# Optimization experiments

Measured on AMD Instinct MI355X. Metric: run time of the kernel, lower is better.

## Reference

```python
import jax, jax.numpy as jnp
import numpy as np

NSAMPLE = 64
RADIUS = 0.05
HMIN = -0.02
HMAX_LIST = (0.01, 0.02, 0.03, 0.04)
BN_EPS = 1e-5
MLP_DIMS = (3, 64, 128, 256)


def setup_inputs() -> dict:
    key = jax.random.key(0)
    ks = jax.random.split(key, 16)
    B, S, N = 2, 1024, 20000
    # points and seeds in a [0,0.5]^3 box so 0.05-radius cylinders are non-empty
    seed_xyz = jax.random.uniform(ks[0], (B, S, 3), dtype=jnp.float32) * 0.5
    pointcloud = jax.random.uniform(ks[1], (B, N, 3), dtype=jnp.float32) * 0.5
    m = jax.random.normal(ks[2], (B, S, 3, 3), dtype=jnp.float32)
    vp_rot, _ = jnp.linalg.qr(m)  # proper-ish random rotations per seed
    inp = {"seed_xyz": seed_xyz, "pointcloud": pointcloud, "vp_rot": vp_rot}
    for i in range(3):
        cin, cout = MLP_DIMS[i], MLP_DIMS[i + 1]
        inp[f"w{i+1}"] = jax.random.normal(ks[3 + i], (cout, cin), dtype=jnp.float32) * (1.0 / np.sqrt(cin))
        inp[f"gamma{i+1}"] = 1.0 + 0.1 * jax.random.normal(ks[6 + i], (cout,), dtype=jnp.float32)
        inp[f"beta{i+1}"] = 0.1 * jax.random.normal(ks[9 + i], (cout,), dtype=jnp.float32)
        inp[f"mean{i+1}"] = 0.1 * jax.random.normal(ks[12 + i], (cout,), dtype=jnp.float32)
        inp[f"var{i+1}"] = jax.random.uniform(ks[15], (cout,), minval=0.5, maxval=1.5, dtype=jnp.float32)
    return inp


def _cylinder_group(rel_rot, hmax):
    # rel_rot: (B, S, N, 3) point coords relative to each seed, in the seed (approach) frame.
    # Cylinder axis = x (approach vector): keep points with hmin < x < hmax and y^2+z^2 < r^2.
    N = rel_rot.shape[2]
    x, y, z = rel_rot[..., 0], rel_rot[..., 1], rel_rot[..., 2]
    mask = (y * y + z * z < RADIUS * RADIUS) & (x > HMIN) & (x < hmax)  # (B,S,N)
    # first NSAMPLE valid indices (ascending), padded with the first valid index (0 if none)
    score = jnp.where(mask, jnp.arange(N, dtype=jnp.int32), N)
    neg_vals, _ = jax.lax.top_k(-score, NSAMPLE)
    idx = -neg_vals  # (B,S,NSAMPLE), value N marks missing
    first = jnp.where(idx[..., :1] >= N, 0, idx[..., :1])
    idx = jnp.where(idx >= N, first, idx)
    return jnp.take_along_axis(rel_rot, idx[..., None], axis=2)  # (B,S,NSAMPLE,3)


def _bn_relu(h, gamma, beta, mean, var):
    inv = gamma / jnp.sqrt(var + BN_EPS)
    s = inv[None, :, None, None]
    b = (beta - mean * inv)[None, :, None, None]
    return jax.nn.relu(h * s + b)


def _forward(seed_xyz, pointcloud, vp_rot, layers):
    B, S, _ = seed_xyz.shape
    D = len(HMAX_LIST)
    rel = pointcloud[:, None, :, :] - seed_xyz[:, :, None, :]        # (B,S,N,3)
    rel_rot = jnp.einsum('bsnc,bscd->bsnd', rel, vp_rot)             # rotate into seed frame (rel @ rot)
    grouped = jnp.stack([_cylinder_group(rel_rot, h) for h in HMAX_LIST], axis=2)  # (B,S,D,ns,3)
    feat = jnp.transpose(grouped, (0, 4, 1, 2, 3)).reshape(B, 3, S * D, NSAMPLE)   # (B,3,S*D,ns)
    for (w, g, be, m, v) in layers:
        feat = _bn_relu(jnp.einsum('oc,bcpn->bopn', w, feat), g, be, m, v)
    vp = jnp.max(feat, axis=-1)                                       # max-pool over nsample
    return vp.reshape(B, -1, S, D)                                    # (B,256,S,D)


def reference(seed_xyz, pointcloud, vp_rot,
              w1, gamma1, beta1, mean1, var1,
              w2, gamma2, beta2, mean2, var2,
              w3, gamma3, beta3, mean3, var3):
    layers = [(w1, gamma1, beta1, mean1, var1),
              (w2, gamma2, beta2, mean2, var2),
              (w3, gamma3, beta3, mean3, var3)]
    return _forward(seed_xyz, pointcloud, vp_rot, layers)
```

## Files before the change

### kernel.cpp

```cpp
#include <hip/hip_runtime.h>

#define NPTS   20000
#define NCHUNK 313

typedef __bf16 bf16x8 __attribute__((ext_vector_type(8)));
typedef float  f32x4  __attribute__((ext_vector_type(4)));

__device__ __forceinline__ unsigned short f2b(float f) {
    __bf16 h = (__bf16)f;
    union { __bf16 h; unsigned short s; } u; u.h = h; return u.s;
}
__device__ __forceinline__ unsigned int pk2(float a, float b) {
    return (unsigned int)f2b(a) | ((unsigned int)f2b(b) << 16);
}
__device__ __forceinline__ bf16x8 pack8v(const float* __restrict__ f) {
    f32x4 a = *(const f32x4*)(f);
    f32x4 c = *(const f32x4*)(f + 4);
    union { unsigned short s[8]; bf16x8 v; } u;
    #pragma unroll
    for (int i = 0; i < 4; ++i) u.s[i]     = f2b(a[i]);
    #pragma unroll
    for (int i = 0; i < 4; ++i) u.s[i + 4] = f2b(c[i]);
    return u.v;
}

#define WS_BINNED  0
#define WS_COUNTS  640000
#define WS_OFFSETS 644096
#define WS_CURSORS 648192

__global__ void zero_kernel(unsigned int* __restrict__ counts,
                            unsigned int* __restrict__ cursors)
{
    int t = blockIdx.x * 256 + threadIdx.x;
    if (t < 1024) { counts[t] = 0; cursors[t] = 0; }
}

__global__ __launch_bounds__(256)
void count_kernel(const float* __restrict__ pointcloud,
                  unsigned int* __restrict__ counts)
{
    int t = blockIdx.x * 256 + threadIdx.x;
    if (t >= 2 * NPTS) return;
    int b = (t >= NPTS) ? 1 : 0;
    const float* p = pointcloud + t * 3;
    int cx = min(7, (int)(p[0] * 16.0f));
    int cy = min(7, (int)(p[1] * 16.0f));
    int cz = min(7, (int)(p[2] * 16.0f));
    int cid = (cz * 8 + cy) * 8 + cx;
    atomicAdd(&counts[b * 512 + cid], 1u);
}

__global__ __launch_bounds__(512)
void prefix_kernel(const unsigned int* __restrict__ counts,
                   unsigned int* __restrict__ offsets,
                   unsigned int* __restrict__ cursors)
{
    __shared__ unsigned int sdat[512];
    int b = blockIdx.x;
    int tid = threadIdx.x;
    unsigned int v = counts[b * 512 + tid];
    sdat[tid] = v;
    __syncthreads();
    #pragma unroll
    for (int off = 1; off < 512; off <<= 1) {
        unsigned int t = 0;
        if (tid >= off) t = sdat[tid - off];
        __syncthreads();
        sdat[tid] += t;
        __syncthreads();
    }
    unsigned int base = b * NPTS + (sdat[tid] - v);
    offsets[b * 512 + tid] = base;
    cursors[b * 512 + tid] = base;
}

__global__ __launch_bounds__(256)
void scatter_kernel(const float* __restrict__ pointcloud,
                    unsigned int* __restrict__ cursors,
                    float4* __restrict__ binned)
{
    int t = blockIdx.x * 256 + threadIdx.x;
    if (t >= 2 * NPTS) return;
    int b = (t >= NPTS) ? 1 : 0;
    int i = t - b * NPTS;
    const float* p = pointcloud + t * 3;
    float x = p[0], y = p[1], z = p[2];
    int cx = min(7, (int)(x * 16.0f));
    int cy = min(7, (int)(y * 16.0f));
    int cz = min(7, (int)(z * 16.0f));
    int cid = (cz * 8 + cy) * 8 + cx;
    unsigned int slot = atomicAdd(&cursors[b * 512 + cid], 1u);
    binned[slot] = make_float4(x, y, z, __int_as_float(i));
}

struct __align__(16) SMemF {
    union {
        struct {
            unsigned int bm[4][640];
            int cstart[64];
            int ccnt[64];
        } a;
        struct {
            unsigned short h1[64][72];
            unsigned short h2[64][136];
        } b;
    } u;
    int    idxs[4][64];
    float  X[4][64][3];
    float2 sb2[128];
    float2 sb3[256];
    float  w1e[64][3];
    float  b1e[64];
};

__global__ __launch_bounds__(256, 2)
void fused_kernel(const float* __restrict__ seed_xyz,
                  const float* __restrict__ pointcloud,
                  const float* __restrict__ vp_rot,
                  const unsigned int* __restrict__ counts,
                  const unsigned int* __restrict__ offsets,
                  const float4* __restrict__ binned,
                  const float* __restrict__ w1,
                  const float* __restrict__ g1,  const float* __restrict__ be1,
                  const float* __restrict__ mn1, const float* __restrict__ vr1,
                  const float* __restrict__ w2,
                  const float* __restrict__ g2,  const float* __restrict__ be2,
                  const float* __restrict__ mn2, const float* __restrict__ vr2,
                  const float* __restrict__ w3,
                  const float* __restrict__ g3,  const float* __restrict__ be3,
                  const float* __restrict__ mn3, const float* __restrict__ vr3,
                  float* __restrict__ out)
{
    __shared__ SMemF sm;
    const int tid = threadIdx.x;
    const int wv  = tid >> 6;
    const int ln  = tid & 63;
    const int q   = ln >> 4;
    const int l15 = ln & 15;

    const int blk = blockIdx.x;
    const int i8  = blk >> 3;
    const int s   = (blk & 7) * 128 + (i8 & 127);
    const int b   = i8 >> 7;
    const int bs  = b * 1024 + s;

    {
        float inv = g3[tid] / sqrtf(vr3[tid] + 1e-5f);
        sm.sb3[tid] = make_float2(inv, be3[tid] - mn3[tid] * inv);
    }
    if (tid < 128) {
        float inv = g2[tid] / sqrtf(vr2[tid] + 1e-5f);
        sm.sb2[tid] = make_float2(inv, be2[tid] - mn2[tid] * inv);
    }
    if (tid < 64) {
        float inv = g1[tid] / sqrtf(vr1[tid] + 1e-5f);
        sm.w1e[tid][0] = inv * w1[tid*3+0];
        sm.w1e[tid][1] = inv * w1[tid*3+1];
        sm.w1e[tid][2] = inv * w1[tid*3+2];
        sm.b1e[tid]    = be1[tid] - mn1[tid] * inv;
    }

    {
        unsigned int* bmp = &sm.u.a.bm[0][0];
        #pragma unroll
        for (int i = 0; i < 10; ++i) bmp[tid + i * 256] = 0;
    }

    const float sx = seed_xyz[bs*3+0];
    const float sy = seed_xyz[bs*3+1];
    const float sz = seed_xyz[bs*3+2];
    const float R00 = vp_rot[bs*9+0], R01 = vp_rot[bs*9+1], R02 = vp_rot[bs*9+2];
    const float R10 = vp_rot[bs*9+3], R11 = vp_rot[bs*9+4], R12 = vp_rot[bs*9+5];
    const float R20 = vp_rot[bs*9+6], R21 = vp_rot[bs*9+7], R22 = vp_rot[bs*9+8];

    const int lx = max(0, (int)floorf((sx - 0.066f) * 16.f));
    const int hx = min(7, (int)floorf((sx + 0.066f) * 16.f));
    const int ly = max(0, (int)floorf((sy - 0.066f) * 16.f));
    const int hy = min(7, (int)floorf((sy + 0.066f) * 16.f));
    const int lz = max(0, (int)floorf((sz - 0.066f) * 16.f));
    const int hz = min(7, (int)floorf((sz + 0.066f) * 16.f));
    const int nx = hx - lx + 1, ny = hy - ly + 1, nz = hz - lz + 1;
    const int ncell = nx * ny * nz;

    if (tid < ncell) {
        int cz = lz + tid / (nx * ny);
        int rem = tid % (nx * ny);
        int cy = ly + rem / nx;
        int cx = lx + rem % nx;
        int cid = (cz * 8 + cy) * 8 + cx;
        sm.u.a.cstart[tid] = (int)offsets[b * 512 + cid];
        sm.u.a.ccnt[tid]   = (int)counts [b * 512 + cid];
    }
    __syncthreads();

    {
        #pragma clang fp contract(off)
        for (int k = wv; k < ncell; k += 4) {
            const int base = sm.u.a.cstart[k];
            const int cnt  = sm.u.a.ccnt[k];
            for (int i = ln; i < cnt; i += 64) {
                float4 pt = binned[base + i];
                float rx = pt.x - sx, ry = pt.y - sy, rz = pt.z - sz;
                float x = (rx*R00 + ry*R10) + rz*R20;
                float y = (rx*R01 + ry*R11) + rz*R21;
                float z = (rx*R02 + ry*R12) + rz*R22;
                if (((y*y + z*z) < 0.0025f) && (x > -0.02f) && (x < 0.04f)) {
                    int n = __float_as_int(pt.w);
                    unsigned int bit = 1u << (n & 31);
                    int wi = n >> 5;
                    if (x < 0.01f) atomicOr(&sm.u.a.bm[0][wi], bit);
                    if (x < 0.02f) atomicOr(&sm.u.a.bm[1][wi], bit);
                    if (x < 0.03f) atomicOr(&sm.u.a.bm[2][wi], bit);
                    atomicOr(&sm.u.a.bm[3][wi], bit);
                }
            }
        }
    }
    __syncthreads();

    {
        const int d = wv;
        int carry = 0;
        for (int r = 0; r < 5 && carry < 64; ++r) {
            int c = r*64 + ln;
            unsigned long long w = 0ULL;
            if (c < NCHUNK)
                w = ((unsigned long long)sm.u.a.bm[d][2*c+1] << 32)
                  |  (unsigned long long)sm.u.a.bm[d][2*c];
            int wc = __popcll(w);
            int incl = wc;
            #pragma unroll
            for (int off = 1; off < 64; off <<= 1) {
                int t = __shfl_up(incl, off);
                if (ln >= off) incl += t;
            }
            int rank  = carry + incl - wc;
            int total = __shfl(incl, 63);
            while (w && rank < 64) {
                int bp = __builtin_ctzll(w);
                w &= w - 1;
                sm.idxs[d][rank] = c*64 + bp;
                ++rank;
            }
            carry += total;
        }
        int cnt = carry < 64 ? carry : 64;
        int first = (cnt > 0) ? sm.idxs[d][0] : 0;
        if (ln >= cnt) sm.idxs[d][ln] = first;
    }
    __syncthreads();

    {
        #pragma clang fp contract(off)
        int n = sm.idxs[wv][ln];
        const float* p = pointcloud + (b*NPTS + n)*3;
        float rx = p[0] - sx, ry = p[1] - sy, rz = p[2] - sz;
        sm.X[wv][ln][0] = (rx*R00 + ry*R10) + rz*R20;
        sm.X[wv][ln][1] = (rx*R01 + ry*R11) + rz*R21;
        sm.X[wv][ln][2] = (rx*R02 + ry*R12) + rz*R22;
    }

    bf16x8 aw2[2][2], aw3[4][4];
    #pragma unroll
    for (int m = 0; m < 2; ++m)
        #pragma unroll
        for (int kk = 0; kk < 2; ++kk)
            aw2[m][kk] = pack8v(w2 + ((wv*2+m)*16 + l15)*64 + kk*32 + q*8);
    #pragma unroll
    for (int m = 0; m < 4; ++m)
        #pragma unroll
        for (int kk = 0; kk < 4; ++kk)
            aw3[m][kk] = pack8v(w3 + ((wv*4+m)*16 + l15)*128 + kk*32 + q*8);

    __syncthreads();

    for (int d = 0; d < 4; ++d) {
        {
            float x0 = sm.X[d][ln][0];
            float x1 = sm.X[d][ln][1];
            float x2 = sm.X[d][ln][2];
            unsigned int pk[8];
            #pragma unroll
            for (int i = 0; i < 8; ++i) {
                int ch = wv*16 + i*2;
                float ha = fmaf(x0, sm.w1e[ch][0],
                           fmaf(x1, sm.w1e[ch][1],
                           fmaf(x2, sm.w1e[ch][2], sm.b1e[ch])));
                float hb = fmaf(x0, sm.w1e[ch+1][0],
                           fmaf(x1, sm.w1e[ch+1][1],
                           fmaf(x2, sm.w1e[ch+1][2], sm.b1e[ch+1])));
                pk[i] = pk2(fmaxf(ha, 0.f), fmaxf(hb, 0.f));
            }
            uint4 u0 = make_uint4(pk[0], pk[1], pk[2], pk[3]);
            uint4 u1 = make_uint4(pk[4], pk[5], pk[6], pk[7]);
            *(uint4*)&sm.u.b.h1[ln][wv*16 + 0] = u0;
            *(uint4*)&sm.u.b.h1[ln][wv*16 + 8] = u1;
        }
        __syncthreads();

        #pragma unroll
        for (int nt = 0; nt < 4; ++nt) {
            int n = nt*16 + l15;
            bf16x8 b0 = *(const bf16x8*)&sm.u.b.h1[n][q*8];
            bf16x8 b1 = *(const bf16x8*)&sm.u.b.h1[n][32 + q*8];
            #pragma unroll
            for (int m = 0; m < 2; ++m) {
                f32x4 acc = {0.f, 0.f, 0.f, 0.f};
                acc = __builtin_amdgcn_mfma_f32_16x16x32_bf16(aw2[m][0], b0, acc, 0, 0, 0);
                acc = __builtin_amdgcn_mfma_f32_16x16x32_bf16(aw2[m][1], b1, acc, 0, 0, 0);
                int ch0 = (wv*2+m)*16 + q*4;
                float2 sb0 = sm.sb2[ch0+0], sb1 = sm.sb2[ch0+1];
                float2 sb2v = sm.sb2[ch0+2], sb3v = sm.sb2[ch0+3];
                uint2 pkk;
                pkk.x = pk2(fmaxf(fmaf(acc[0], sb0.x, sb0.y), 0.f),
                            fmaxf(fmaf(acc[1], sb1.x, sb1.y), 0.f));
                pkk.y = pk2(fmaxf(fmaf(acc[2], sb2v.x, sb2v.y), 0.f),
                            fmaxf(fmaf(acc[3], sb3v.x, sb3v.y), 0.f));
                *(uint2*)&sm.u.b.h2[n][ch0] = pkk;
            }
        }
        __syncthreads();

        {
            float rm[4][4];
            #pragma unroll
            for (int m = 0; m < 4; ++m)
                #pragma unroll
                for (int r = 0; r < 4; ++r) rm[m][r] = 0.f;

            #pragma unroll
            for (int nt = 0; nt < 4; ++nt) {
                int n = nt*16 + l15;
                bf16x8 bb0 = *(const bf16x8*)&sm.u.b.h2[n][ 0 + q*8];
                bf16x8 bb1 = *(const bf16x8*)&sm.u.b.h2[n][32 + q*8];
                bf16x8 bb2 = *(const bf16x8*)&sm.u.b.h2[n][64 + q*8];
                bf16x8 bb3 = *(const bf16x8*)&sm.u.b.h2[n][96 + q*8];
                #pragma unroll
                for (int m = 0; m < 4; ++m) {
                    f32x4 acc = {0.f, 0.f, 0.f, 0.f};
                    acc = __builtin_amdgcn_mfma_f32_16x16x32_bf16(aw3[m][0], bb0, acc, 0, 0, 0);
                    acc = __builtin_amdgcn_mfma_f32_16x16x32_bf16(aw3[m][1], bb1, acc, 0, 0, 0);
                    acc = __builtin_amdgcn_mfma_f32_16x16x32_bf16(aw3[m][2], bb2, acc, 0, 0, 0);
                    acc = __builtin_amdgcn_mfma_f32_16x16x32_bf16(aw3[m][3], bb3, acc, 0, 0, 0);
                    int ch0 = (wv*4+m)*16 + q*4;
                    #pragma unroll
                    for (int r = 0; r < 4; ++r) {
                        float2 sb = sm.sb3[ch0 + r];
                        float v = fmaxf(fmaf(acc[r], sb.x, sb.y), 0.f);
                        rm[m][r] = fmaxf(rm[m][r], v);
                    }
                }
            }
            #pragma unroll
            for (int m = 0; m < 4; ++m) {
                #pragma unroll
                for (int r = 0; r < 4; ++r) {
                    float v = rm[m][r];
                    v = fmaxf(v, __shfl_xor(v, 1));
                    v = fmaxf(v, __shfl_xor(v, 2));
                    v = fmaxf(v, __shfl_xor(v, 4));
                    v = fmaxf(v, __shfl_xor(v, 8));
                    if (l15 == 0) {
                        int ch = (wv*4+m)*16 + q*4 + r;
                        out[((b*256 + ch)*1024 + s)*4 + d] = v;
                    }
                }
            }
        }
        __syncthreads();
    }
}

extern "C" void kernel_launch(void* const* d_in, const int* in_sizes, int n_in,
                              void* d_out, int out_size, void* d_ws, size_t ws_size,
                              hipStream_t stream) {
    (void)in_sizes; (void)n_in; (void)out_size; (void)ws_size;
    const float* seed = (const float*)d_in[0];
    const float* pc   = (const float*)d_in[1];
    const float* rot  = (const float*)d_in[2];
    const float* w1   = (const float*)d_in[3];
    const float* g1   = (const float*)d_in[4];
    const float* be1  = (const float*)d_in[5];
    const float* mn1  = (const float*)d_in[6];
    const float* vr1  = (const float*)d_in[7];
    const float* w2   = (const float*)d_in[8];
    const float* g2   = (const float*)d_in[9];
    const float* be2  = (const float*)d_in[10];
    const float* mn2  = (const float*)d_in[11];
    const float* vr2  = (const float*)d_in[12];
    const float* w3   = (const float*)d_in[13];
    const float* g3   = (const float*)d_in[14];
    const float* be3  = (const float*)d_in[15];
    const float* mn3  = (const float*)d_in[16];
    const float* vr3  = (const float*)d_in[17];

    char* ws = (char*)d_ws;
    float4*       binned  = (float4*)(ws + WS_BINNED);
    unsigned int* counts  = (unsigned int*)(ws + WS_COUNTS);
    unsigned int* offsets = (unsigned int*)(ws + WS_OFFSETS);
    unsigned int* cursors = (unsigned int*)(ws + WS_CURSORS);

    zero_kernel   <<<dim3(4),    dim3(256), 0, stream>>>(counts, cursors);
    count_kernel  <<<dim3(157),  dim3(256), 0, stream>>>(pc, counts);
    prefix_kernel <<<dim3(2),    dim3(512), 0, stream>>>(counts, offsets, cursors);
    scatter_kernel<<<dim3(157),  dim3(256), 0, stream>>>(pc, cursors, binned);
    fused_kernel  <<<dim3(2048), dim3(256), 0, stream>>>(
        seed, pc, rot, counts, offsets, binned,
        w1, g1, be1, mn1, vr1,
        w2, g2, be2, mn2, vr2,
        w3, g3, be3, mn3, vr3,
        (float*)d_out);
}
```

Before: 243.4 us.

## Merge binning into one kernel and overlap layer-1 with layer-3 compute

Replaces the four binning kernels (zero, count, prefix, scatter) with a single per-batch 1024-thread kernel that builds the histogram, scan and scatter in shared memory, removing three launches and the global atomics. In the fused kernel, the gathered-point rotation and layer-1 MLP for the next cylinder depth are computed inside the current depth's loop, after its layer-3 MFMAs. This drops the X staging buffer and one barrier per depth. The trade-off is that binning now runs on only 2 blocks, which serialises 20000 points per block, and shared-atomic slot order is nondeterministic, as it already was with the global atomics.

```diff
diff --git a/kernel.cpp b/kernel.cpp
--- a/kernel.cpp
+++ b/kernel.cpp
@@ -27,71 +27,58 @@
 #define WS_BINNED  0
 #define WS_COUNTS  640000
 #define WS_OFFSETS 644096
-#define WS_CURSORS 648192
-
-__global__ void zero_kernel(unsigned int* __restrict__ counts,
-                            unsigned int* __restrict__ cursors)
+
+__global__ __launch_bounds__(1024)
+void bin_kernel(const float* __restrict__ pointcloud,
+                unsigned int* __restrict__ counts,
+                unsigned int* __restrict__ offsets,
+                float4* __restrict__ binned)
 {
-    int t = blockIdx.x * 256 + threadIdx.x;
-    if (t < 1024) { counts[t] = 0; cursors[t] = 0; }
-}
-
-__global__ __launch_bounds__(256)
-void count_kernel(const float* __restrict__ pointcloud,
-                  unsigned int* __restrict__ counts)
-{
-    int t = blockIdx.x * 256 + threadIdx.x;
-    if (t >= 2 * NPTS) return;
-    int b = (t >= NPTS) ? 1 : 0;
-    const float* p = pointcloud + t * 3;
-    int cx = min(7, (int)(p[0] * 16.0f));
-    int cy = min(7, (int)(p[1] * 16.0f));
-    int cz = min(7, (int)(p[2] * 16.0f));
-    int cid = (cz * 8 + cy) * 8 + cx;
-    atomicAdd(&counts[b * 512 + cid], 1u);
-}
-
-__global__ __launch_bounds__(512)
-void prefix_kernel(const unsigned int* __restrict__ counts,
-                   unsigned int* __restrict__ offsets,
-                   unsigned int* __restrict__ cursors)
-{
-    __shared__ unsigned int sdat[512];
-    int b = blockIdx.x;
-    int tid = threadIdx.x;
-    unsigned int v = counts[b * 512 + tid];
-    sdat[tid] = v;
+    __shared__ unsigned int hist[512];
+    __shared__ unsigned int scanv[512];
+    __shared__ unsigned int cur[512];
+    const int b   = blockIdx.x;
+    const int tid = threadIdx.x;
+
+    if (tid < 512) hist[tid] = 0;
+    __syncthreads();
+
+    const float* base = pointcloud + b * NPTS * 3;
+    for (int i = tid; i < NPTS; i += 1024) {
+        float x = base[i*3+0], y = base[i*3+1], z = base[i*3+2];
+        int cx = min(7, (int)(x * 16.0f));
+        int cy = min(7, (int)(y * 16.0f));
+        int cz = min(7, (int)(z * 16.0f));
+        atomicAdd(&hist[(cz * 8 + cy) * 8 + cx], 1u);
+    }
+    __syncthreads();
+
+    if (tid < 512) scanv[tid] = hist[tid];
     __syncthreads();
     #pragma unroll
     for (int off = 1; off < 512; off <<= 1) {
-        unsigned int t = 0;
-        if (tid >= off) t = sdat[tid - off];
+        unsigned int v = 0;
+        if (tid < 512 && tid >= off) v = scanv[tid - off];
         __syncthreads();
-        sdat[tid] += t;
+        if (tid < 512) scanv[tid] += v;
         __syncthreads();
     }
-    unsigned int base = b * NPTS + (sdat[tid] - v);
-    offsets[b * 512 + tid] = base;
-    cursors[b * 512 + tid] = base;
-}
-
-__global__ __launch_bounds__(256)
-void scatter_kernel(const float* __restrict__ pointcloud,
-                    unsigned int* __restrict__ cursors,
-                    float4* __restrict__ binned)
-{
-    int t = blockIdx.x * 256 + threadIdx.x;
-    if (t >= 2 * NPTS) return;
-    int b = (t >= NPTS) ? 1 : 0;
-    int i = t - b * NPTS;
-    const float* p = pointcloud + t * 3;
-    float x = p[0], y = p[1], z = p[2];
-    int cx = min(7, (int)(x * 16.0f));
-    int cy = min(7, (int)(y * 16.0f));
-    int cz = min(7, (int)(z * 16.0f));
-    int cid = (cz * 8 + cy) * 8 + cx;
-    unsigned int slot = atomicAdd(&cursors[b * 512 + cid], 1u);
-    binned[slot] = make_float4(x, y, z, __int_as_float(i));
+    if (tid < 512) {
+        unsigned int excl = scanv[tid] - hist[tid];
+        offsets[b * 512 + tid] = b * NPTS + excl;
+        counts [b * 512 + tid] = hist[tid];
+        cur[tid] = excl;
+    }
+    __syncthreads();
+
+    for (int i = tid; i < NPTS; i += 1024) {
+        float x = base[i*3+0], y = base[i*3+1], z = base[i*3+2];
+        int cx = min(7, (int)(x * 16.0f));
+        int cy = min(7, (int)(y * 16.0f));
+        int cz = min(7, (int)(z * 16.0f));
+        unsigned int slot = atomicAdd(&cur[(cz * 8 + cy) * 8 + cx], 1u);
+        binned[b * NPTS + slot] = make_float4(x, y, z, __int_as_float(i));
+    }
 }
 
 struct __align__(16) SMemF {
@@ -107,7 +94,6 @@
         } b;
     } u;
     int    idxs[4][64];
-    float  X[4][64][3];
     float2 sb2[128];
     float2 sb3[256];
     float  w1e[64][3];
@@ -249,17 +235,6 @@
         int first = (cnt > 0) ? sm.idxs[d][0] : 0;
         if (ln >= cnt) sm.idxs[d][ln] = first;
     }
-    __syncthreads();
-
-    {
-        #pragma clang fp contract(off)
-        int n = sm.idxs[wv][ln];
-        const float* p = pointcloud + (b*NPTS + n)*3;
-        float rx = p[0] - sx, ry = p[1] - sy, rz = p[2] - sz;
-        sm.X[wv][ln][0] = (rx*R00 + ry*R10) + rz*R20;
-        sm.X[wv][ln][1] = (rx*R01 + ry*R11) + rz*R21;
-        sm.X[wv][ln][2] = (rx*R02 + ry*R12) + rz*R22;
-    }
 
     bf16x8 aw2[2][2], aw3[4][4];
     #pragma unroll
@@ -275,30 +250,37 @@
 
     __syncthreads();
 
+    auto do_l1 = [&](int d) {
+        int n = sm.idxs[d][ln];
+        const float* p = pointcloud + (b*NPTS + n)*3;
+        float x0, x1, x2;
+        {
+            #pragma clang fp contract(off)
+            float rx = p[0] - sx, ry = p[1] - sy, rz = p[2] - sz;
+            x0 = (rx*R00 + ry*R10) + rz*R20;
+            x1 = (rx*R01 + ry*R11) + rz*R21;
+            x2 = (rx*R02 + ry*R12) + rz*R22;
+        }
+        unsigned int pk[8];
+        #pragma unroll
+        for (int i = 0; i < 8; ++i) {
+            int ch = wv*16 + i*2;
+            float ha = fmaf(x0, sm.w1e[ch][0],
+                       fmaf(x1, sm.w1e[ch][1],
+                       fmaf(x2, sm.w1e[ch][2], sm.b1e[ch])));
+            float hb = fmaf(x0, sm.w1e[ch+1][0],
+                       fmaf(x1, sm.w1e[ch+1][1],
+                       fmaf(x2, sm.w1e[ch+1][2], sm.b1e[ch+1])));
+            pk[i] = pk2(fmaxf(ha, 0.f), fmaxf(hb, 0.f));
+        }
+        *(uint4*)&sm.u.b.h1[ln][wv*16 + 0] = make_uint4(pk[0], pk[1], pk[2], pk[3]);
+        *(uint4*)&sm.u.b.h1[ln][wv*16 + 8] = make_uint4(pk[4], pk[5], pk[6], pk[7]);
+    };
+
+    do_l1(0);
+    __syncthreads();
+
     for (int d = 0; d < 4; ++d) {
-        {
-            float x0 = sm.X[d][ln][0];
-            float x1 = sm.X[d][ln][1];
-            float x2 = sm.X[d][ln][2];
-            unsigned int pk[8];
-            #pragma unroll
-            for (int i = 0; i < 8; ++i) {
-                int ch = wv*16 + i*2;
-                float ha = fmaf(x0, sm.w1e[ch][0],
-                           fmaf(x1, sm.w1e[ch][1],
-                           fmaf(x2, sm.w1e[ch][2], sm.b1e[ch])));
-                float hb = fmaf(x0, sm.w1e[ch+1][0],
-                           fmaf(x1, sm.w1e[ch+1][1],
-                           fmaf(x2, sm.w1e[ch+1][2], sm.b1e[ch+1])));
-                pk[i] = pk2(fmaxf(ha, 0.f), fmaxf(hb, 0.f));
-            }
-            uint4 u0 = make_uint4(pk[0], pk[1], pk[2], pk[3]);
-            uint4 u1 = make_uint4(pk[4], pk[5], pk[6], pk[7]);
-            *(uint4*)&sm.u.b.h1[ln][wv*16 + 0] = u0;
-            *(uint4*)&sm.u.b.h1[ln][wv*16 + 8] = u1;
-        }
-        __syncthreads();
-
         #pragma unroll
         for (int nt = 0; nt < 4; ++nt) {
             int n = nt*16 + l15;
@@ -352,6 +334,9 @@
                     }
                 }
             }
+
+            if (d < 3) do_l1(d + 1);
+
             #pragma unroll
             for (int m = 0; m < 4; ++m) {
                 #pragma unroll
@@ -368,7 +353,7 @@
                 }
             }
         }
-        __syncthreads();
+        if (d < 3) __syncthreads();
     }
 }
 
@@ -399,13 +384,9 @@
     float4*       binned  = (float4*)(ws + WS_BINNED);
     unsigned int* counts  = (unsigned int*)(ws + WS_COUNTS);
     unsigned int* offsets = (unsigned int*)(ws + WS_OFFSETS);
-    unsigned int* cursors = (unsigned int*)(ws + WS_CURSORS);
-
-    zero_kernel   <<<dim3(4),    dim3(256), 0, stream>>>(counts, cursors);
-    count_kernel  <<<dim3(157),  dim3(256), 0, stream>>>(pc, counts);
-    prefix_kernel <<<dim3(2),    dim3(512), 0, stream>>>(counts, offsets, cursors);
-    scatter_kernel<<<dim3(157),  dim3(256), 0, stream>>>(pc, cursors, binned);
-    fused_kernel  <<<dim3(2048), dim3(256), 0, stream>>>(
+
+    bin_kernel  <<<dim3(2),    dim3(1024), 0, stream>>>(pc, counts, offsets, binned);
+    fused_kernel<<<dim3(2048), dim3(256),  0, stream>>>(
         seed, pc, rot, counts, offsets, binned,
         w1, g1, be1, mn1, vr1,
         w2, g2, be2, mn2, vr2,
```

New measurement: 251.3 us. +3.2%, slower.
